# Performance work log

Hardware: AMD Instinct MI355X
Metric: run time of the kernel (lower is better)

The kernel has to match this reference:

```python
import jax, jax.numpy as jnp
import numpy as np

# geomloss SamplesLoss('sinkhorn', p=1, blur=0.05, diameter=10) equivalents
BLUR = 0.05        # final epsilon (p=1 -> eps = blur**1)
DIAMETER = 10.0    # starting epsilon for eps-scaling
SCALING = 0.5      # geomloss default annealing ratio
N_POINTS = 32
SPACE_DIM = 8      # emb_dim // n_points = 256 // 32


def _eps_schedule():
    eps, e = [], DIAMETER
    while e > BLUR:
        eps.append(e)
        e *= SCALING
    eps.append(BLUR)
    return eps  # static python list -> unrolled under jit


def _cost(x, y):
    # p=1 ground cost: euclidean distance. x:[B,n,d], y:[B,m,d] -> [B,n,m]
    sq = (jnp.sum(x * x, -1)[:, :, None] + jnp.sum(y * y, -1)[:, None, :]
          - 2.0 * jnp.einsum('bnd,bmd->bnm', x, y))
    return jnp.sqrt(jnp.maximum(sq, 0.0) + 1e-8)


def _softmin(eps, C, h):
    # -eps * logsumexp_j( log(1/n) + (h_j - C_ij)/eps ), uniform weights
    n = C.shape[-1]
    return -eps * jax.nn.logsumexp((h[:, None, :] - C) / eps - jnp.log(n), axis=-1)


def _sinkhorn_div(x, y):
    # Debiased Sinkhorn divergence with epsilon scaling (log-domain, symmetric
    # averaged updates, as in geomloss). x, y: [B, n, d] -> [B]
    C_xy = _cost(x, y)
    C_yx = jnp.swapaxes(C_xy, 1, 2)
    C_xx = _cost(x, x)
    C_yy = _cost(y, y)
    B, n, _ = C_xy.shape
    z = jnp.zeros((B, n), x.dtype)
    f_ab, g_ba, f_aa, g_bb = z, z, z, z
    for eps in _eps_schedule():
        ft = _softmin(eps, C_xy, g_ba)
        gt = _softmin(eps, C_yx, f_ab)
        fat = _softmin(eps, C_xx, f_aa)
        gbt = _softmin(eps, C_yy, g_bb)
        f_ab = 0.5 * (f_ab + ft)
        g_ba = 0.5 * (g_ba + gt)
        f_aa = 0.5 * (f_aa + fat)
        g_bb = 0.5 * (g_bb + gbt)
    return jnp.mean(f_ab - f_aa, axis=1) + jnp.mean(g_ba - g_bb, axis=1)


def _encode(x, edge_index, W):
    # simple mean-aggregation GCN layer standing in for the generic encoder
    src, dst = edge_index[0], edge_index[1]
    N = x.shape[0]
    agg = jax.ops.segment_sum(x[src], dst, num_segments=N)
    deg = jax.ops.segment_sum(jnp.ones((src.shape[0],), x.dtype), dst, num_segments=N)
    return (agg / jnp.maximum(deg, 1.0)[:, None]) @ W  # [N, emb_dim]


def setup_inputs() -> dict:
    key = jax.random.key(0)
    k1, k2, k3, k4, k5 = jax.random.split(key, 5)
    N, F, EMB = 100000, 128, 256
    return {
        'x': jax.random.normal(k1, (N, F), dtype=jnp.float32),
        'edge_index': jax.random.randint(k2, (2, 1600000), 0, N, dtype=jnp.int64),
        'edges_pos': jax.random.randint(k3, (2, 30000), 0, N, dtype=jnp.int64),
        'edges_neg': jax.random.randint(k4, (2, 30000), 0, N, dtype=jnp.int64),
        'W': jax.random.normal(k5, (F, EMB), dtype=jnp.float32) * (1.0 / np.sqrt(F)),
    }


def reference(x, edge_index, edges_pos, edges_neg, W):
    z = _encode(x, edge_index, W)

    def energy(edges):  # -score_pairs = sinkhorn divergence
        zx = z[edges[0]].reshape(-1, N_POINTS, SPACE_DIM)
        zy = z[edges[1]].reshape(-1, N_POINTS, SPACE_DIM)
        return _sinkhorn_div(zx, zy)

    pos_energy = energy(edges_pos)
    neg_energy = energy(edges_neg)
    margin = jnp.maximum(1.0 - neg_energy, 0.0)
    return jnp.mean(pos_energy ** 2) + jnp.mean(margin ** 2)
```

## Files before the change

### kernel.cpp

```cpp
#include <hip/hip_runtime.h>
#include <hip/hip_bf16.h>


__global__ __launch_bounds__(256) void sge_count(
    const int* __restrict__ dst, int* __restrict__ cnt, int nE) {
  int e = blockIdx.x * 256 + threadIdx.x;
  if (e >= nE) return;
  atomicAdd(&cnt[dst[e]], 1);
}

__global__ __launch_bounds__(256) void sge_blocksum(
    const int* __restrict__ cnt, int* __restrict__ bsum, int N) {
  int i = blockIdx.x * 256 + threadIdx.x;
  int v = (i < N) ? cnt[i] : 0;
#pragma unroll
  for (int o = 1; o < 64; o <<= 1) v += __shfl_xor(v, o);
  __shared__ int ws[4];
  int lane = threadIdx.x & 63, wid = threadIdx.x >> 6;
  if (lane == 0) ws[wid] = v;
  __syncthreads();
  if (threadIdx.x == 0)
    bsum[blockIdx.x] = ws[0] + ws[1] + ws[2] + ws[3];
}

__global__ __launch_bounds__(64) void sge_scan_top(
    int* __restrict__ bsum, int* __restrict__ offs, int nb, int N, int nE) {
  int lane = threadIdx.x;
  int carry = 0;
  for (int base = 0; base < nb; base += 64) {
    int i = base + lane;
    int v = (i < nb) ? bsum[i] : 0;
    int s = v;
#pragma unroll
    for (int o = 1; o < 64; o <<= 1) {
      int t = __shfl_up(s, o);
      if (lane >= o) s += t;
    }
    if (i < nb) bsum[i] = carry + s - v;
    carry += __shfl(s, 63);
  }
  if (lane == 0) offs[N] = nE;
}

__global__ __launch_bounds__(256) void sge_scan_block(
    const int* __restrict__ cnt, const int* __restrict__ bsum,
    int* __restrict__ offs, int* __restrict__ pos, int N) {
  int i = blockIdx.x * 256 + threadIdx.x;
  int v = (i < N) ? cnt[i] : 0;
  int lane = threadIdx.x & 63, wid = threadIdx.x >> 6;
  int s = v;
#pragma unroll
  for (int o = 1; o < 64; o <<= 1) {
    int t = __shfl_up(s, o);
    if (lane >= o) s += t;
  }
  __shared__ int ws[4];
  if (lane == 63) ws[wid] = s;
  __syncthreads();
  int wbase = 0;
  for (int w = 0; w < wid; ++w) wbase += ws[w];
  if (i < N) {
    int o = bsum[blockIdx.x] + wbase + s - v;
    offs[i] = o;
    pos[i] = o;
  }
}

__global__ __launch_bounds__(256) void sge_fill(
    const int* __restrict__ src, const int* __restrict__ dst,
    int* __restrict__ pos, int* __restrict__ sorted_src, int nE) {
  int e = blockIdx.x * 256 + threadIdx.x;
  if (e >= nE) return;
  int p = atomicAdd(&pos[dst[e]], 1);
  sorted_src[p] = src[e];
}

__global__ __launch_bounds__(256) void sge_gather(
    const float* __restrict__ x, const int* __restrict__ sorted_src,
    const int* __restrict__ offs, float* __restrict__ agg, int N) {
  int node = blockIdx.x * 4 + (threadIdx.x >> 6);
  int lane = threadIdx.x & 63;
  int h = lane >> 5;
  int c4 = (lane & 31) << 2;
  if (node >= N) return;
  int e0 = offs[node], e1 = offs[node + 1];
  float4 A = {0.f, 0.f, 0.f, 0.f}, B = {0.f, 0.f, 0.f, 0.f};
  int e = e0 + h;
  for (; e + 2 < e1; e += 4) {
    int s0 = sorted_src[e];
    int s1 = sorted_src[e + 2];
    float4 v0 = *(const float4*)&x[(size_t)s0 * 128 + c4];
    float4 v1 = *(const float4*)&x[(size_t)s1 * 128 + c4];
    A.x += v0.x; A.y += v0.y; A.z += v0.z; A.w += v0.w;
    B.x += v1.x; B.y += v1.y; B.z += v1.z; B.w += v1.w;
  }
  if (e < e1) {
    float4 v0 = *(const float4*)&x[(size_t)sorted_src[e] * 128 + c4];
    A.x += v0.x; A.y += v0.y; A.z += v0.z; A.w += v0.w;
  }
  float4 S;
  S.x = A.x + B.x; S.y = A.y + B.y; S.z = A.z + B.z; S.w = A.w + B.w;
  S.x += __shfl_xor(S.x, 32);
  S.y += __shfl_xor(S.y, 32);
  S.z += __shfl_xor(S.z, 32);
  S.w += __shfl_xor(S.w, 32);
  if (h == 0) {
    float inv = 1.0f / fmaxf((float)(e1 - e0), 1.0f);
    float4 r;
    r.x = S.x * inv; r.y = S.y * inv; r.z = S.z * inv; r.w = S.w * inv;
    *(float4*)&agg[(size_t)node * 128 + c4] = r;
  }
}

__global__ __launch_bounds__(256) void sge_gemm(
    const float* __restrict__ agg, const float* __restrict__ W,
    float* __restrict__ z) {
  __shared__ float xs[32][128];
  int n0 = blockIdx.x * 32;
  int t = threadIdx.x;
#pragma unroll
  for (int i = 0; i < 16; ++i) {
    int idx = t + i * 256;
    int r = idx >> 7;
    int c = idx & 127;
    xs[r][c] = agg[(long long)(n0 + r) * 128 + c];
  }
  __syncthreads();
  int wv = t >> 6, lane = t & 63;
  int r0 = wv * 8;
  float acc[8][4];
#pragma unroll
  for (int r = 0; r < 8; ++r)
#pragma unroll
    for (int q = 0; q < 4; ++q) acc[r][q] = 0.f;
  for (int k = 0; k < 128; k += 4) {
    float4 xv[8];
#pragma unroll
    for (int r = 0; r < 8; ++r) xv[r] = *(const float4*)&xs[r0 + r][k];
#pragma unroll
    for (int kk = 0; kk < 4; ++kk) {
      const float* Wr = W + (k + kk) * 256 + lane;
      float w0 = Wr[0], w1 = Wr[64], w2 = Wr[128], w3 = Wr[192];
#pragma unroll
      for (int r = 0; r < 8; ++r) {
        float xk = (kk == 0) ? xv[r].x
                 : (kk == 1) ? xv[r].y
                 : (kk == 2) ? xv[r].z : xv[r].w;
        acc[r][0] = fmaf(xk, w0, acc[r][0]);
        acc[r][1] = fmaf(xk, w1, acc[r][1]);
        acc[r][2] = fmaf(xk, w2, acc[r][2]);
        acc[r][3] = fmaf(xk, w3, acc[r][3]);
      }
    }
  }
#pragma unroll
  for (int r = 0; r < 8; ++r) {
    float* zr = z + (long long)(n0 + r0 + r) * 256 + lane;
#pragma unroll
    for (int q = 0; q < 4; ++q) zr[q * 64] = acc[r][q];
  }
}

template <int CTRL>
__device__ __forceinline__ float dpp_max(float x) {
  int r = __builtin_amdgcn_update_dpp(__float_as_int(x), __float_as_int(x),
                                      CTRL, 0xF, 0xF, false);
  return fmaxf(x, __int_as_float(r));
}
template <int CTRL>
__device__ __forceinline__ float dpp_add(float x) {
  int r = __builtin_amdgcn_update_dpp(0, __float_as_int(x), CTRL, 0xF, 0xF, true);
  return x + __int_as_float(r);
}

__global__ __launch_bounds__(256, 4) void sge_energy(
    const float* __restrict__ z, const int* __restrict__ ep,
    const int* __restrict__ en, float* __restrict__ partial, int nP) {
  __shared__ __align__(16) float Ebuf[2][2][64];
  __shared__ __align__(16) float Nbuf[2][2][64];
  __shared__ float red[2][2];

  int t = threadIdx.x;
  int pl = t >> 7;
  int tp = t & 127;
  int w = tp >> 6;
  int l = tp & 63;
  int row = l & 31;
  int own = l & 32;

  int pair = blockIdx.x * 2 + pl;
  bool isPos = pair < nP;
  int idx = isPos ? pair : pair - nP;
  const int* E = isPos ? ep : en;
  int na = E[idx], nb = E[idx + nP];

  const float* zrow = z + (size_t)(own ? nb : na) * 256 + row * 8;
  float4 r0 = ((const float4*)zrow)[0];
  float4 r1 = ((const float4*)zrow)[1];
  float xr[8];
  xr[0] = r0.x; xr[1] = r0.y; xr[2] = r0.z; xr[3] = r0.w;
  xr[4] = r1.x; xr[5] = r1.y; xr[6] = r1.z; xr[7] = r1.w;

  float nself = xr[0] * xr[0];
  nself = fmaf(xr[1], xr[1], nself); nself = fmaf(xr[2], xr[2], nself);
  nself = fmaf(xr[3], xr[3], nself); nself = fmaf(xr[4], xr[4], nself);
  nself = fmaf(xr[5], xr[5], nself); nself = fmaf(xr[6], xr[6], nself);
  nself = fmaf(xr[7], xr[7], nself);
  Nbuf[pl][w][l] = nself;
  __builtin_amdgcn_wave_barrier();

  bool colIsX = (w == 0) ? (own != 0) : (own == 0);
  const float4* zc = (const float4*)(z + (size_t)(colIsX ? na : nb) * 256);
  int rb = (w == 0) ? (own ^ 32) : own;
  const float* Nw = Nbuf[pl][w] + rb;

  const float RLNE = 1.44269504088896340736f;
  const float LN2 = 0.69314718055994530942f;
  const float LN32 = 3.46573590279972654709f;
  const float K20 = RLNE / 10.0f;
  const float NK28 = -RLNE / 0.05f;

  float C[32], V[32];
#pragma unroll
  for (int jq = 0; jq < 8; ++jq) {
    float4 nj4 = ((const float4*)Nw)[jq];
    float4 a[8];
#pragma unroll
    for (int k = 0; k < 4; ++k) {
      a[2 * k] = zc[8 * jq + 2 * k];
      a[2 * k + 1] = zc[8 * jq + 2 * k + 1];
    }
#pragma unroll
    for (int k = 0; k < 4; ++k) {
      int j = jq * 4 + k;
      float4 a0 = a[2 * k], a1 = a[2 * k + 1];
      float d = xr[0] * a0.x;
      d = fmaf(xr[1], a0.y, d); d = fmaf(xr[2], a0.z, d);
      d = fmaf(xr[3], a0.w, d); d = fmaf(xr[4], a1.x, d);
      d = fmaf(xr[5], a1.y, d); d = fmaf(xr[6], a1.z, d);
      d = fmaf(xr[7], a1.w, d);
      float nj = (k == 0) ? nj4.x : (k == 1) ? nj4.y : (k == 2) ? nj4.z : nj4.w;
      float sq = fmaf(-2.0f, d, nself + nj);
      float Cv = __builtin_amdgcn_sqrtf(fmaxf(sq, 0.0f) + 1e-8f);
      C[j] = Cv;
      V[j] = __builtin_amdgcn_exp2f(-Cv * K20);
    }
  }

  float* Ew = Ebuf[pl][w];

  float P = 0.0f;
  float epsv = 10.0f;

#pragma unroll 1
  for (int it = 0; it < 9; ++it) {
    float eps = (it == 8) ? 0.05f : epsv;
    float k2 = RLNE / eps;
    float eln2 = eps * LN2;
    float c32 = eps * LN32;

    if (it == 8) {
#pragma unroll
      for (int j = 0; j < 32; ++j)
        V[j] = __builtin_amdgcn_exp2f(C[j] * NK28);
    } else if (it > 0) {
#pragma unroll
      for (int j = 0; j < 32; ++j) V[j] *= V[j];
    }

    float mOwn, mRead;
    if (it >= 7) {
      float m = P;
      m = dpp_max<0x111>(m);
      m = dpp_max<0x112>(m);
      m = dpp_max<0x114>(m);
      m = dpp_max<0x118>(m);
      m = dpp_max<0x142>(m);
      float g0 = __int_as_float(__builtin_amdgcn_readlane(__float_as_int(m), 31));
      float g1 = __int_as_float(__builtin_amdgcn_readlane(__float_as_int(m), 63));
      mOwn = own ? g1 : g0;
      mRead = (w == 0) ? (own ? g0 : g1) : mOwn;
    } else {
      mOwn = 0.0f;
      mRead = 0.0f;
    }

    Ew[l] = __builtin_amdgcn_exp2f((P - mOwn) * k2);
    __builtin_amdgcn_wave_barrier();

    float s0 = 0.f, s1 = 0.f, s2 = 0.f, s3 = 0.f;
#pragma unroll
    for (int jq = 0; jq < 8; ++jq) {
      float4 Ev = ((const float4*)(Ew + rb))[jq];
      s0 = fmaf(Ev.x, V[4 * jq + 0], s0);
      s1 = fmaf(Ev.y, V[4 * jq + 1], s1);
      s2 = fmaf(Ev.z, V[4 * jq + 2], s2);
      s3 = fmaf(Ev.w, V[4 * jq + 3], s3);
    }
    float s = fmaxf((s0 + s1) + (s2 + s3), 1e-37f);
    __builtin_amdgcn_wave_barrier();

    P = 0.5f * (P + (c32 - mRead - eln2 * __builtin_amdgcn_logf(s)));
    epsv *= 0.5f;
  }

  float d = P;
  d = dpp_add<0x111>(d);
  d = dpp_add<0x112>(d);
  d = dpp_add<0x114>(d);
  d = dpp_add<0x118>(d);
  d = dpp_add<0x142>(d);
  float s31 = __int_as_float(__builtin_amdgcn_readlane(__float_as_int(d), 31));
  float s63 = __int_as_float(__builtin_amdgcn_readlane(__float_as_int(d), 63));
  if (l == 0) red[pl][w] = s31 + s63;
  __syncthreads();
  if (t == 0) {
    float tot = 0.0f;
#pragma unroll
    for (int q = 0; q < 2; ++q) {
      int pr = blockIdx.x * 2 + q;
      float e = (red[q][0] - red[q][1]) * (1.0f / 32.0f);
      float term;
      if (pr < nP) {
        term = e * e;
      } else {
        float mm = fmaxf(1.0f - e, 0.0f);
        term = mm * mm;
      }
      tot += term;
    }
    partial[blockIdx.x] = tot;
  }
}

__global__ __launch_bounds__(1024) void sge_reduce(
    const float* __restrict__ partial, int n, float invnP,
    float* __restrict__ out) {
  __shared__ float ws[16];
  float s = 0.0f;
  for (int i = threadIdx.x; i < n; i += 1024) s += partial[i];
#pragma unroll
  for (int o = 1; o < 64; o <<= 1) s += __shfl_xor(s, o);
  if ((threadIdx.x & 63) == 0) ws[threadIdx.x >> 6] = s;
  __syncthreads();
  if (threadIdx.x == 0) {
    float tt = 0.0f;
#pragma unroll
    for (int q = 0; q < 16; ++q) tt += ws[q];
    out[0] = tt * invnP;
  }
}

extern "C" void kernel_launch(void* const* d_in, const int* in_sizes, int n_in,
                              void* d_out, int out_size, void* d_ws, size_t ws_size,
                              hipStream_t stream) {
  const float* x  = (const float*)d_in[0];
  const int*   ei = (const int*)d_in[1];
  const int*   ep = (const int*)d_in[2];
  const int*   en = (const int*)d_in[3];
  const float* W  = (const float*)d_in[4];
  float* out = (float*)d_out;

  int N  = in_sizes[0] / 128;
  int nE = in_sizes[1] / 2;
  int nP = in_sizes[2] / 2;

  size_t zBytes   = (size_t)N * 256 * sizeof(float);
  size_t aggBytes = (size_t)N * 128 * sizeof(float);
  if (ws_size < zBytes + aggBytes) return;

  char* ws = (char*)d_ws;
  float* z   = (float*)ws;
  float* agg = (float*)(ws + zBytes);

  int* cnt        = (int*)ws;
  int* offs       = cnt + N;
  int* pos        = offs + N + 1;
  int* bsum       = pos + N;
  int* sorted_src = bsum + 4096;

  float* partial = agg;

  int nb = (N + 255) / 256;

  hipMemsetAsync(cnt, 0, (size_t)N * sizeof(int), stream);

  const int* src = ei;
  const int* dst = ei + nE;

  int eb = (nE + 255) / 256;
  sge_count<<<eb, 256, 0, stream>>>(dst, cnt, nE);
  sge_blocksum<<<nb, 256, 0, stream>>>(cnt, bsum, N);
  sge_scan_top<<<1, 64, 0, stream>>>(bsum, offs, nb, N, nE);
  sge_scan_block<<<nb, 256, 0, stream>>>(cnt, bsum, offs, pos, N);
  sge_fill<<<eb, 256, 0, stream>>>(src, dst, pos, sorted_src, nE);
  sge_gather<<<(N + 3) / 4, 256, 0, stream>>>(x, sorted_src, offs, agg, N);

  sge_gemm<<<(N + 31) / 32, 256, 0, stream>>>(agg, W, z);

  sge_energy<<<nP, 256, 0, stream>>>(z, ep, en, partial, nP);
  sge_reduce<<<1, 1024, 0, stream>>>(partial, nP, 1.0f / (float)nP, out);
}
```

Before: 690.9 us.

## Process one pair per wave computing both cross and self kernels per lane

```diff
diff --git a/kernel.cpp b/kernel.cpp
--- a/kernel.cpp
+++ b/kernel.cpp
@@ -172,25 +172,30 @@
   int r = __builtin_amdgcn_update_dpp(0, __float_as_int(x), CTRL, 0xF, 0xF, true);
   return x + __int_as_float(r);
 }
+__device__ __forceinline__ float rdlane(float v, int lane) {
+  return __int_as_float(__builtin_amdgcn_readlane(__float_as_int(v), lane));
+}
 
 __global__ __launch_bounds__(256, 4) void sge_energy(
     const float* __restrict__ z, const int* __restrict__ ep,
     const int* __restrict__ en, float* __restrict__ partial, int nP) {
-  __shared__ __align__(16) float Ebuf[2][2][64];
-  __shared__ __align__(16) float Nbuf[2][2][64];
-  __shared__ float red[2][2];
+  __shared__ __align__(16) float EbA[4][64];
+  __shared__ __align__(16) float EbB[4][64];
+  __shared__ __align__(16) float Nbuf[4][64];
+  __shared__ float red[4];
 
   int t = threadIdx.x;
-  int pl = t >> 7;
-  int tp = t & 127;
-  int w = tp >> 6;
-  int l = tp & 63;
+  int wv = t >> 6;
+  int l = t & 63;
   int row = l & 31;
   int own = l & 32;
 
-  int pair = blockIdx.x * 2 + pl;
-  bool isPos = pair < nP;
-  int idx = isPos ? pair : pair - nP;
+  int n2 = 2 * nP;
+  int pair = blockIdx.x * 4 + wv;
+  bool live = pair < n2;
+  int pr = live ? pair : 0;
+  bool isPos = pr < nP;
+  int idx = isPos ? pr : pr - nP;
   const int* E = isPos ? ep : en;
   int na = E[idx], nb = E[idx + nP];
 
@@ -206,50 +211,57 @@
   nself = fmaf(xr[3], xr[3], nself); nself = fmaf(xr[4], xr[4], nself);
   nself = fmaf(xr[5], xr[5], nself); nself = fmaf(xr[6], xr[6], nself);
   nself = fmaf(xr[7], xr[7], nself);
-  Nbuf[pl][w][l] = nself;
+  Nbuf[wv][l] = nself;
   __builtin_amdgcn_wave_barrier();
 
-  bool colIsX = (w == 0) ? (own != 0) : (own == 0);
-  const float4* zc = (const float4*)(z + (size_t)(colIsX ? na : nb) * 256);
-  int rb = (w == 0) ? (own ^ 32) : own;
-  const float* Nw = Nbuf[pl][w] + rb;
+  const float4* zcA = (const float4*)(z + (size_t)(own ? na : nb) * 256);
+  const float4* zcB = (const float4*)(z + (size_t)(own ? nb : na) * 256);
+  int rbA = own ^ 32;
+  int rbB = own;
+  const float* NwA = Nbuf[wv] + rbA;
+  const float* NwB = Nbuf[wv] + rbB;
 
   const float RLNE = 1.44269504088896340736f;
   const float LN2 = 0.69314718055994530942f;
   const float LN32 = 3.46573590279972654709f;
   const float K20 = RLNE / 10.0f;
-  const float NK28 = -RLNE / 0.05f;
-
-  float C[32], V[32];
+
+  float VA[32], VB[32];
 #pragma unroll
   for (int jq = 0; jq < 8; ++jq) {
-    float4 nj4 = ((const float4*)Nw)[jq];
-    float4 a[8];
-#pragma unroll
-    for (int k = 0; k < 4; ++k) {
-      a[2 * k] = zc[8 * jq + 2 * k];
-      a[2 * k + 1] = zc[8 * jq + 2 * k + 1];
-    }
+    float4 njA = ((const float4*)NwA)[jq];
+    float4 njB = ((const float4*)NwB)[jq];
 #pragma unroll
     for (int k = 0; k < 4; ++k) {
       int j = jq * 4 + k;
-      float4 a0 = a[2 * k], a1 = a[2 * k + 1];
-      float d = xr[0] * a0.x;
-      d = fmaf(xr[1], a0.y, d); d = fmaf(xr[2], a0.z, d);
-      d = fmaf(xr[3], a0.w, d); d = fmaf(xr[4], a1.x, d);
-      d = fmaf(xr[5], a1.y, d); d = fmaf(xr[6], a1.z, d);
-      d = fmaf(xr[7], a1.w, d);
-      float nj = (k == 0) ? nj4.x : (k == 1) ? nj4.y : (k == 2) ? nj4.z : nj4.w;
-      float sq = fmaf(-2.0f, d, nself + nj);
-      float Cv = __builtin_amdgcn_sqrtf(fmaxf(sq, 0.0f) + 1e-8f);
-      C[j] = Cv;
-      V[j] = __builtin_amdgcn_exp2f(-Cv * K20);
-    }
-  }
-
-  float* Ew = Ebuf[pl][w];
-
-  float P = 0.0f;
+      float4 a0 = zcA[2 * j];
+      float4 a1 = zcA[2 * j + 1];
+      float4 b0 = zcB[2 * j];
+      float4 b1 = zcB[2 * j + 1];
+      float dA = xr[0] * a0.x;
+      float dB = xr[0] * b0.x;
+      dA = fmaf(xr[1], a0.y, dA); dB = fmaf(xr[1], b0.y, dB);
+      dA = fmaf(xr[2], a0.z, dA); dB = fmaf(xr[2], b0.z, dB);
+      dA = fmaf(xr[3], a0.w, dA); dB = fmaf(xr[3], b0.w, dB);
+      dA = fmaf(xr[4], a1.x, dA); dB = fmaf(xr[4], b1.x, dB);
+      dA = fmaf(xr[5], a1.y, dA); dB = fmaf(xr[5], b1.y, dB);
+      dA = fmaf(xr[6], a1.z, dA); dB = fmaf(xr[6], b1.z, dB);
+      dA = fmaf(xr[7], a1.w, dA); dB = fmaf(xr[7], b1.w, dB);
+      float nA = (k == 0) ? njA.x : (k == 1) ? njA.y : (k == 2) ? njA.z : njA.w;
+      float nB = (k == 0) ? njB.x : (k == 1) ? njB.y : (k == 2) ? njB.z : njB.w;
+      float sqA = fmaf(-2.0f, dA, nself + nA);
+      float sqB = fmaf(-2.0f, dB, nself + nB);
+      float CA = __builtin_amdgcn_sqrtf(fmaxf(sqA, 0.0f) + 1e-8f);
+      float CB = __builtin_amdgcn_sqrtf(fmaxf(sqB, 0.0f) + 1e-8f);
+      VA[j] = __builtin_amdgcn_exp2f(-CA * K20);
+      VB[j] = __builtin_amdgcn_exp2f(-CB * K20);
+    }
+  }
+
+  float* EA = EbA[wv];
+  float* EB = EbB[wv];
+
+  float PA = 0.0f, PB = 0.0f;
   float epsv = 10.0f;
 
 #pragma unroll 1
@@ -261,76 +273,88 @@
 
     if (it == 8) {
 #pragma unroll
-      for (int j = 0; j < 32; ++j)
-        V[j] = __builtin_amdgcn_exp2f(C[j] * NK28);
+      for (int j = 0; j < 32; ++j) {
+        VA[j] = __builtin_amdgcn_exp2f(1.5625f * __builtin_amdgcn_logf(VA[j]));
+        VB[j] = __builtin_amdgcn_exp2f(1.5625f * __builtin_amdgcn_logf(VB[j]));
+      }
     } else if (it > 0) {
 #pragma unroll
-      for (int j = 0; j < 32; ++j) V[j] *= V[j];
-    }
-
-    float mOwn, mRead;
+      for (int j = 0; j < 32; ++j) {
+        VA[j] *= VA[j];
+        VB[j] *= VB[j];
+      }
+    }
+
+    float mOwnA, mReadA, mOwnB;
     if (it >= 7) {
-      float m = P;
-      m = dpp_max<0x111>(m);
-      m = dpp_max<0x112>(m);
-      m = dpp_max<0x114>(m);
-      m = dpp_max<0x118>(m);
-      m = dpp_max<0x142>(m);
-      float g0 = __int_as_float(__builtin_amdgcn_readlane(__float_as_int(m), 31));
-      float g1 = __int_as_float(__builtin_amdgcn_readlane(__float_as_int(m), 63));
-      mOwn = own ? g1 : g0;
-      mRead = (w == 0) ? (own ? g0 : g1) : mOwn;
+      float mA = PA, mB = PB;
+      mA = dpp_max<0x111>(mA); mB = dpp_max<0x111>(mB);
+      mA = dpp_max<0x112>(mA); mB = dpp_max<0x112>(mB);
+      mA = dpp_max<0x114>(mA); mB = dpp_max<0x114>(mB);
+      mA = dpp_max<0x118>(mA); mB = dpp_max<0x118>(mB);
+      mA = dpp_max<0x142>(mA); mB = dpp_max<0x142>(mB);
+      float gA0 = rdlane(mA, 31), gA1 = rdlane(mA, 63);
+      float gB0 = rdlane(mB, 31), gB1 = rdlane(mB, 63);
+      mOwnA = own ? gA1 : gA0;
+      mReadA = own ? gA0 : gA1;
+      mOwnB = own ? gB1 : gB0;
     } else {
-      mOwn = 0.0f;
-      mRead = 0.0f;
-    }
-
-    Ew[l] = __builtin_amdgcn_exp2f((P - mOwn) * k2);
+      mOwnA = mReadA = 0.0f;
+      mOwnB = 0.0f;
+    }
+
+    EA[l] = __builtin_amdgcn_exp2f((PA - mOwnA) * k2);
+    EB[l] = __builtin_amdgcn_exp2f((PB - mOwnB) * k2);
     __builtin_amdgcn_wave_barrier();
 
-    float s0 = 0.f, s1 = 0.f, s2 = 0.f, s3 = 0.f;
+    float sA0 = 0.f, sA1 = 0.f, sA2 = 0.f, sA3 = 0.f;
+    float sB0 = 0.f, sB1 = 0.f, sB2 = 0.f, sB3 = 0.f;
 #pragma unroll
     for (int jq = 0; jq < 8; ++jq) {
-      float4 Ev = ((const float4*)(Ew + rb))[jq];
-      s0 = fmaf(Ev.x, V[4 * jq + 0], s0);
-      s1 = fmaf(Ev.y, V[4 * jq + 1], s1);
-      s2 = fmaf(Ev.z, V[4 * jq + 2], s2);
-      s3 = fmaf(Ev.w, V[4 * jq + 3], s3);
-    }
-    float s = fmaxf((s0 + s1) + (s2 + s3), 1e-37f);
+      float4 EvA = ((const float4*)(EA + rbA))[jq];
+      float4 EvB = ((const float4*)(EB + rbB))[jq];
+      sA0 = fmaf(EvA.x, VA[4 * jq + 0], sA0);
+      sB0 = fmaf(EvB.x, VB[4 * jq + 0], sB0);
+      sA1 = fmaf(EvA.y, VA[4 * jq + 1], sA1);
+      sB1 = fmaf(EvB.y, VB[4 * jq + 1], sB1);
+      sA2 = fmaf(EvA.z, VA[4 * jq + 2], sA2);
+      sB2 = fmaf(EvB.z, VB[4 * jq + 2], sB2);
+      sA3 = fmaf(EvA.w, VA[4 * jq + 3], sA3);
+      sB3 = fmaf(EvB.w, VB[4 * jq + 3], sB3);
+    }
+    float sA = fmaxf((sA0 + sA1) + (sA2 + sA3), 1e-37f);
+    float sB = fmaxf((sB0 + sB1) + (sB2 + sB3), 1e-37f);
     __builtin_amdgcn_wave_barrier();
 
-    P = 0.5f * (P + (c32 - mRead - eln2 * __builtin_amdgcn_logf(s)));
+    PA = 0.5f * (PA + (c32 - mReadA - eln2 * __builtin_amdgcn_logf(sA)));
+    PB = 0.5f * (PB + (c32 - mOwnB - eln2 * __builtin_amdgcn_logf(sB)));
     epsv *= 0.5f;
   }
 
-  float d = P;
-  d = dpp_add<0x111>(d);
-  d = dpp_add<0x112>(d);
-  d = dpp_add<0x114>(d);
-  d = dpp_add<0x118>(d);
-  d = dpp_add<0x142>(d);
-  float s31 = __int_as_float(__builtin_amdgcn_readlane(__float_as_int(d), 31));
-  float s63 = __int_as_float(__builtin_amdgcn_readlane(__float_as_int(d), 63));
-  if (l == 0) red[pl][w] = s31 + s63;
-  __syncthreads();
-  if (t == 0) {
-    float tot = 0.0f;
-#pragma unroll
-    for (int q = 0; q < 2; ++q) {
-      int pr = blockIdx.x * 2 + q;
-      float e = (red[q][0] - red[q][1]) * (1.0f / 32.0f);
-      float term;
-      if (pr < nP) {
+  float dA = PA, dB = PB;
+  dA = dpp_add<0x111>(dA); dB = dpp_add<0x111>(dB);
+  dA = dpp_add<0x112>(dA); dB = dpp_add<0x112>(dB);
+  dA = dpp_add<0x114>(dA); dB = dpp_add<0x114>(dB);
+  dA = dpp_add<0x118>(dA); dB = dpp_add<0x118>(dB);
+  dA = dpp_add<0x142>(dA); dB = dpp_add<0x142>(dB);
+  float sumA = rdlane(dA, 31) + rdlane(dA, 63);
+  float sumB = rdlane(dB, 31) + rdlane(dB, 63);
+  if (l == 0) {
+    float term = 0.0f;
+    if (live) {
+      float e = (sumA - sumB) * (1.0f / 32.0f);
+      if (isPos) {
         term = e * e;
       } else {
         float mm = fmaxf(1.0f - e, 0.0f);
         term = mm * mm;
       }
-      tot += term;
-    }
-    partial[blockIdx.x] = tot;
-  }
+    }
+    red[wv] = term;
+  }
+  __syncthreads();
+  if (t == 0)
+    partial[blockIdx.x] = (red[0] + red[1]) + (red[2] + red[3]);
 }
 
 __global__ __launch_bounds__(1024) void sge_reduce(
@@ -398,6 +422,7 @@
 
   sge_gemm<<<(N + 31) / 32, 256, 0, stream>>>(agg, W, z);
 
-  sge_energy<<<nP, 256, 0, stream>>>(z, ep, en, partial, nP);
-  sge_reduce<<<1, 1024, 0, stream>>>(partial, nP, 1.0f / (float)nP, out);
-}
+  int eblocks = (2 * nP + 3) / 4;
+  sge_energy<<<eblocks, 256, 0, stream>>>(z, ep, en, partial, nP);
+  sge_reduce<<<1, 1024, 0, stream>>>(partial, eblocks, 1.0f / (float)nP, out);
+}
```

After: 1.313 ms. 90.1% more time.

## Split Sinkhorn rows across lane pairs and drop stored cost matrix

Applied to the files above, without the earlier changes.

```diff
diff --git a/kernel.cpp b/kernel.cpp
--- a/kernel.cpp
+++ b/kernel.cpp
@@ -172,21 +172,25 @@
   int r = __builtin_amdgcn_update_dpp(0, __float_as_int(x), CTRL, 0xF, 0xF, true);
   return x + __int_as_float(r);
 }
+__device__ __forceinline__ float rdlane(float v, int lane) {
+  return __int_as_float(__builtin_amdgcn_readlane(__float_as_int(v), lane));
+}
 
 __global__ __launch_bounds__(256, 4) void sge_energy(
     const float* __restrict__ z, const int* __restrict__ ep,
     const int* __restrict__ en, float* __restrict__ partial, int nP) {
-  __shared__ __align__(16) float Ebuf[2][2][64];
-  __shared__ __align__(16) float Nbuf[2][2][64];
+  __shared__ __align__(16) float EbA[4][32];
+  __shared__ __align__(16) float EbB[4][32];
+  __shared__ __align__(16) float Nbuf[4][64];
   __shared__ float red[2][2];
 
   int t = threadIdx.x;
-  int pl = t >> 7;
-  int tp = t & 127;
-  int w = tp >> 6;
-  int l = tp & 63;
-  int row = l & 31;
-  int own = l & 32;
+  int wv = t >> 6;
+  int pl = wv >> 1;
+  int w = wv & 1;
+  int l = t & 63;
+  int row = l >> 1;
+  int ch = l & 1;
 
   int pair = blockIdx.x * 2 + pl;
   bool isPos = pair < nP;
@@ -194,62 +198,80 @@
   const int* E = isPos ? ep : en;
   int na = E[idx], nb = E[idx + nP];
 
-  const float* zrow = z + (size_t)(own ? nb : na) * 256 + row * 8;
-  float4 r0 = ((const float4*)zrow)[0];
-  float4 r1 = ((const float4*)zrow)[1];
-  float xr[8];
-  xr[0] = r0.x; xr[1] = r0.y; xr[2] = r0.z; xr[3] = r0.w;
-  xr[4] = r1.x; xr[5] = r1.y; xr[6] = r1.z; xr[7] = r1.w;
-
-  float nself = xr[0] * xr[0];
-  nself = fmaf(xr[1], xr[1], nself); nself = fmaf(xr[2], xr[2], nself);
-  nself = fmaf(xr[3], xr[3], nself); nself = fmaf(xr[4], xr[4], nself);
-  nself = fmaf(xr[5], xr[5], nself); nself = fmaf(xr[6], xr[6], nself);
-  nself = fmaf(xr[7], xr[7], nself);
-  Nbuf[pl][w][l] = nself;
+  const float* zx = z + (size_t)na * 256;
+  const float* zy = z + (size_t)nb * 256;
+
+  float xrow[8], yrow[8];
+  {
+    float4 a0 = ((const float4*)(zx + row * 8))[0];
+    float4 a1 = ((const float4*)(zx + row * 8))[1];
+    float4 b0 = ((const float4*)(zy + row * 8))[0];
+    float4 b1 = ((const float4*)(zy + row * 8))[1];
+    xrow[0] = a0.x; xrow[1] = a0.y; xrow[2] = a0.z; xrow[3] = a0.w;
+    xrow[4] = a1.x; xrow[5] = a1.y; xrow[6] = a1.z; xrow[7] = a1.w;
+    yrow[0] = b0.x; yrow[1] = b0.y; yrow[2] = b0.z; yrow[3] = b0.w;
+    yrow[4] = b1.x; yrow[5] = b1.y; yrow[6] = b1.z; yrow[7] = b1.w;
+  }
+  float nxr = xrow[0] * xrow[0];
+  float nyr = yrow[0] * yrow[0];
+#pragma unroll
+  for (int d = 1; d < 8; ++d) {
+    nxr = fmaf(xrow[d], xrow[d], nxr);
+    nyr = fmaf(yrow[d], yrow[d], nyr);
+  }
+  Nbuf[wv][row] = nxr;
+  Nbuf[wv][32 + row] = nyr;
   __builtin_amdgcn_wave_barrier();
 
-  bool colIsX = (w == 0) ? (own != 0) : (own == 0);
-  const float4* zc = (const float4*)(z + (size_t)(colIsX ? na : nb) * 256);
-  int rb = (w == 0) ? (own ^ 32) : own;
-  const float* Nw = Nbuf[pl][w] + rb;
+  const float4* colsA = (const float4*)((w == 0) ? zy : zx);
+  const float4* colsB = (const float4*)((w == 0) ? zx : zy);
+  const float* NcA = (w == 0) ? (Nbuf[wv] + 32) : Nbuf[wv];
+  const float* NcB = (w == 0) ? Nbuf[wv] : (Nbuf[wv] + 32);
 
   const float RLNE = 1.44269504088896340736f;
   const float LN2 = 0.69314718055994530942f;
   const float LN32 = 3.46573590279972654709f;
   const float K20 = RLNE / 10.0f;
-  const float NK28 = -RLNE / 0.05f;
-
-  float C[32], V[32];
-#pragma unroll
-  for (int jq = 0; jq < 8; ++jq) {
-    float4 nj4 = ((const float4*)Nw)[jq];
-    float4 a[8];
+
+  float VA[16], VB[16];
+#pragma unroll
+  for (int jq = 0; jq < 4; ++jq) {
+    float4 nA4 = ((const float4*)(NcA + ch * 16))[jq];
+    float4 nB4 = ((const float4*)(NcB + ch * 16))[jq];
 #pragma unroll
     for (int k = 0; k < 4; ++k) {
-      a[2 * k] = zc[8 * jq + 2 * k];
-      a[2 * k + 1] = zc[8 * jq + 2 * k + 1];
-    }
-#pragma unroll
-    for (int k = 0; k < 4; ++k) {
-      int j = jq * 4 + k;
-      float4 a0 = a[2 * k], a1 = a[2 * k + 1];
-      float d = xr[0] * a0.x;
-      d = fmaf(xr[1], a0.y, d); d = fmaf(xr[2], a0.z, d);
-      d = fmaf(xr[3], a0.w, d); d = fmaf(xr[4], a1.x, d);
-      d = fmaf(xr[5], a1.y, d); d = fmaf(xr[6], a1.z, d);
-      d = fmaf(xr[7], a1.w, d);
-      float nj = (k == 0) ? nj4.x : (k == 1) ? nj4.y : (k == 2) ? nj4.z : nj4.w;
-      float sq = fmaf(-2.0f, d, nself + nj);
-      float Cv = __builtin_amdgcn_sqrtf(fmaxf(sq, 0.0f) + 1e-8f);
-      C[j] = Cv;
-      V[j] = __builtin_amdgcn_exp2f(-Cv * K20);
-    }
-  }
-
-  float* Ew = Ebuf[pl][w];
-
-  float P = 0.0f;
+      int jj = jq * 4 + k;
+      int j = ch * 16 + jj;
+      float4 a0 = colsA[2 * j];
+      float4 a1 = colsA[2 * j + 1];
+      float4 b0 = colsB[2 * j];
+      float4 b1 = colsB[2 * j + 1];
+      float dA = xrow[0] * a0.x;
+      float dB = yrow[0] * b0.x;
+      dA = fmaf(xrow[1], a0.y, dA); dB = fmaf(yrow[1], b0.y, dB);
+      dA = fmaf(xrow[2], a0.z, dA); dB = fmaf(yrow[2], b0.z, dB);
+      dA = fmaf(xrow[3], a0.w, dA); dB = fmaf(yrow[3], b0.w, dB);
+      dA = fmaf(xrow[4], a1.x, dA); dB = fmaf(yrow[4], b1.x, dB);
+      dA = fmaf(xrow[5], a1.y, dA); dB = fmaf(yrow[5], b1.y, dB);
+      dA = fmaf(xrow[6], a1.z, dA); dB = fmaf(yrow[6], b1.z, dB);
+      dA = fmaf(xrow[7], a1.w, dA); dB = fmaf(yrow[7], b1.w, dB);
+      float nA = (k == 0) ? nA4.x : (k == 1) ? nA4.y : (k == 2) ? nA4.z : nA4.w;
+      float nB = (k == 0) ? nB4.x : (k == 1) ? nB4.y : (k == 2) ? nB4.z : nB4.w;
+      float sqA = fmaf(-2.0f, dA, nxr + nA);
+      float sqB = fmaf(-2.0f, dB, nyr + nB);
+      float CA = __builtin_amdgcn_sqrtf(fmaxf(sqA, 0.0f) + 1e-8f);
+      float CB = __builtin_amdgcn_sqrtf(fmaxf(sqB, 0.0f) + 1e-8f);
+      VA[jj] = __builtin_amdgcn_exp2f(-CA * K20);
+      VB[jj] = __builtin_amdgcn_exp2f(-CB * K20);
+    }
+  }
+
+  float* EAw = EbA[wv];
+  float* EBw = EbB[wv];
+  const float* ErdA = (w == 0) ? EBw : EAw;
+  const float* ErdB = (w == 0) ? EAw : EBw;
+
+  float PA = 0.0f, PB = 0.0f;
   float epsv = 10.0f;
 
 #pragma unroll 1
@@ -261,65 +283,82 @@
 
     if (it == 8) {
 #pragma unroll
-      for (int j = 0; j < 32; ++j)
-        V[j] = __builtin_amdgcn_exp2f(C[j] * NK28);
+      for (int j = 0; j < 16; ++j) {
+        VA[j] = __builtin_amdgcn_exp2f(1.5625f * __builtin_amdgcn_logf(VA[j]));
+        VB[j] = __builtin_amdgcn_exp2f(1.5625f * __builtin_amdgcn_logf(VB[j]));
+      }
     } else if (it > 0) {
 #pragma unroll
-      for (int j = 0; j < 32; ++j) V[j] *= V[j];
-    }
-
-    float mOwn, mRead;
+      for (int j = 0; j < 16; ++j) {
+        VA[j] *= VA[j];
+        VB[j] *= VB[j];
+      }
+    }
+
+    float mA, mB;
     if (it >= 7) {
-      float m = P;
-      m = dpp_max<0x111>(m);
-      m = dpp_max<0x112>(m);
-      m = dpp_max<0x114>(m);
-      m = dpp_max<0x118>(m);
-      m = dpp_max<0x142>(m);
-      float g0 = __int_as_float(__builtin_amdgcn_readlane(__float_as_int(m), 31));
-      float g1 = __int_as_float(__builtin_amdgcn_readlane(__float_as_int(m), 63));
-      mOwn = own ? g1 : g0;
-      mRead = (w == 0) ? (own ? g0 : g1) : mOwn;
+      float a = PA, b = PB;
+      a = dpp_max<0x111>(a); b = dpp_max<0x111>(b);
+      a = dpp_max<0x112>(a); b = dpp_max<0x112>(b);
+      a = dpp_max<0x114>(a); b = dpp_max<0x114>(b);
+      a = dpp_max<0x118>(a); b = dpp_max<0x118>(b);
+      a = dpp_max<0x142>(a); b = dpp_max<0x142>(b);
+      mA = fmaxf(rdlane(a, 31), rdlane(a, 63));
+      mB = fmaxf(rdlane(b, 31), rdlane(b, 63));
     } else {
-      mOwn = 0.0f;
-      mRead = 0.0f;
-    }
-
-    Ew[l] = __builtin_amdgcn_exp2f((P - mOwn) * k2);
+      mA = 0.0f;
+      mB = 0.0f;
+    }
+
+    EAw[row] = __builtin_amdgcn_exp2f((PA - mA) * k2);
+    EBw[row] = __builtin_amdgcn_exp2f((PB - mB) * k2);
     __builtin_amdgcn_wave_barrier();
 
-    float s0 = 0.f, s1 = 0.f, s2 = 0.f, s3 = 0.f;
-#pragma unroll
-    for (int jq = 0; jq < 8; ++jq) {
-      float4 Ev = ((const float4*)(Ew + rb))[jq];
-      s0 = fmaf(Ev.x, V[4 * jq + 0], s0);
-      s1 = fmaf(Ev.y, V[4 * jq + 1], s1);
-      s2 = fmaf(Ev.z, V[4 * jq + 2], s2);
-      s3 = fmaf(Ev.w, V[4 * jq + 3], s3);
-    }
-    float s = fmaxf((s0 + s1) + (s2 + s3), 1e-37f);
+    float sA0 = 0.f, sA1 = 0.f, sA2 = 0.f, sA3 = 0.f;
+    float sB0 = 0.f, sB1 = 0.f, sB2 = 0.f, sB3 = 0.f;
+#pragma unroll
+    for (int jq = 0; jq < 4; ++jq) {
+      float4 EvA = ((const float4*)(ErdA + ch * 16))[jq];
+      float4 EvB = ((const float4*)(ErdB + ch * 16))[jq];
+      sA0 = fmaf(EvA.x, VA[4 * jq + 0], sA0);
+      sB0 = fmaf(EvB.x, VB[4 * jq + 0], sB0);
+      sA1 = fmaf(EvA.y, VA[4 * jq + 1], sA1);
+      sB1 = fmaf(EvB.y, VB[4 * jq + 1], sB1);
+      sA2 = fmaf(EvA.z, VA[4 * jq + 2], sA2);
+      sB2 = fmaf(EvB.z, VB[4 * jq + 2], sB2);
+      sA3 = fmaf(EvA.w, VA[4 * jq + 3], sA3);
+      sB3 = fmaf(EvB.w, VB[4 * jq + 3], sB3);
+    }
+    float sA = (sA0 + sA1) + (sA2 + sA3);
+    float sB = (sB0 + sB1) + (sB2 + sB3);
+    sA = dpp_add<0xB1>(sA);
+    sB = dpp_add<0xB1>(sB);
+    sA = fmaxf(sA, 1e-37f);
+    sB = fmaxf(sB, 1e-37f);
     __builtin_amdgcn_wave_barrier();
 
-    P = 0.5f * (P + (c32 - mRead - eln2 * __builtin_amdgcn_logf(s)));
+    float mUA = (w == 0) ? mB : mA;
+    float mUB = (w == 0) ? mA : mB;
+    PA = 0.5f * (PA + (c32 - mUA - eln2 * __builtin_amdgcn_logf(sA)));
+    PB = 0.5f * (PB + (c32 - mUB - eln2 * __builtin_amdgcn_logf(sB)));
     epsv *= 0.5f;
   }
 
-  float d = P;
+  float d = PA + PB;
   d = dpp_add<0x111>(d);
   d = dpp_add<0x112>(d);
   d = dpp_add<0x114>(d);
   d = dpp_add<0x118>(d);
   d = dpp_add<0x142>(d);
-  float s31 = __int_as_float(__builtin_amdgcn_readlane(__float_as_int(d), 31));
-  float s63 = __int_as_float(__builtin_amdgcn_readlane(__float_as_int(d), 63));
-  if (l == 0) red[pl][w] = s31 + s63;
+  float sum = rdlane(d, 31) + rdlane(d, 63);
+  if (l == 0) red[pl][w] = sum;
   __syncthreads();
   if (t == 0) {
     float tot = 0.0f;
 #pragma unroll
     for (int q = 0; q < 2; ++q) {
       int pr = blockIdx.x * 2 + q;
-      float e = (red[q][0] - red[q][1]) * (1.0f / 32.0f);
+      float e = (red[q][0] - red[q][1]) * (1.0f / 64.0f);
       float term;
       if (pr < nP) {
         term = e * e;
@@ -398,6 +437,7 @@
 
   sge_gemm<<<(N + 31) / 32, 256, 0, stream>>>(agg, W, z);
 
-  sge_energy<<<nP, 256, 0, stream>>>(z, ep, en, partial, nP);
-  sge_reduce<<<1, 1024, 0, stream>>>(partial, nP, 1.0f / (float)nP, out);
-}
+  int eblocks = nP;
+  sge_energy<<<eblocks, 256, 0, stream>>>(z, ep, en, partial, nP);
+  sge_reduce<<<1, 1024, 0, stream>>>(partial, eblocks, 1.0f / (float)nP, out);
+}
```

After: 871.8 us. 1.26x slower.

## Fuse neighbor mean-aggregation gather into the GEMM shared-memory tile load

Applied to the files above, without the earlier changes.

```diff
diff --git a/kernel.cpp b/kernel.cpp
--- a/kernel.cpp
+++ b/kernel.cpp
@@ -75,57 +75,41 @@
   sorted_src[p] = src[e];
 }
 
-__global__ __launch_bounds__(256) void sge_gather(
+__global__ __launch_bounds__(256) void sge_gemm(
     const float* __restrict__ x, const int* __restrict__ sorted_src,
-    const int* __restrict__ offs, float* __restrict__ agg, int N) {
-  int node = blockIdx.x * 4 + (threadIdx.x >> 6);
-  int lane = threadIdx.x & 63;
-  int h = lane >> 5;
-  int c4 = (lane & 31) << 2;
-  if (node >= N) return;
-  int e0 = offs[node], e1 = offs[node + 1];
-  float4 A = {0.f, 0.f, 0.f, 0.f}, B = {0.f, 0.f, 0.f, 0.f};
-  int e = e0 + h;
-  for (; e + 2 < e1; e += 4) {
-    int s0 = sorted_src[e];
-    int s1 = sorted_src[e + 2];
-    float4 v0 = *(const float4*)&x[(size_t)s0 * 128 + c4];
-    float4 v1 = *(const float4*)&x[(size_t)s1 * 128 + c4];
-    A.x += v0.x; A.y += v0.y; A.z += v0.z; A.w += v0.w;
-    B.x += v1.x; B.y += v1.y; B.z += v1.z; B.w += v1.w;
-  }
-  if (e < e1) {
-    float4 v0 = *(const float4*)&x[(size_t)sorted_src[e] * 128 + c4];
-    A.x += v0.x; A.y += v0.y; A.z += v0.z; A.w += v0.w;
-  }
-  float4 S;
-  S.x = A.x + B.x; S.y = A.y + B.y; S.z = A.z + B.z; S.w = A.w + B.w;
-  S.x += __shfl_xor(S.x, 32);
-  S.y += __shfl_xor(S.y, 32);
-  S.z += __shfl_xor(S.z, 32);
-  S.w += __shfl_xor(S.w, 32);
-  if (h == 0) {
-    float inv = 1.0f / fmaxf((float)(e1 - e0), 1.0f);
-    float4 r;
-    r.x = S.x * inv; r.y = S.y * inv; r.z = S.z * inv; r.w = S.w * inv;
-    *(float4*)&agg[(size_t)node * 128 + c4] = r;
-  }
-}
-
-__global__ __launch_bounds__(256) void sge_gemm(
-    const float* __restrict__ agg, const float* __restrict__ W,
+    const int* __restrict__ offs, const float* __restrict__ W,
     float* __restrict__ z) {
   __shared__ float xs[32][128];
   int n0 = blockIdx.x * 32;
   int t = threadIdx.x;
-#pragma unroll
-  for (int i = 0; i < 16; ++i) {
-    int idx = t + i * 256;
-    int r = idx >> 7;
-    int c = idx & 127;
-    xs[r][c] = agg[(long long)(n0 + r) * 128 + c];
-  }
-  __syncthreads();
+
+  {
+    int r = t >> 3;
+    int c0 = (t & 7) << 4;
+    int node = n0 + r;
+    int e0 = offs[node], e1 = offs[node + 1];
+    float4 a0 = {0.f, 0.f, 0.f, 0.f}, a1 = {0.f, 0.f, 0.f, 0.f};
+    float4 a2 = {0.f, 0.f, 0.f, 0.f}, a3 = {0.f, 0.f, 0.f, 0.f};
+    for (int e = e0; e < e1; ++e) {
+      int s = sorted_src[e];
+      const float4* xr = (const float4*)&x[(size_t)s * 128 + c0];
+      float4 v0 = xr[0], v1 = xr[1], v2 = xr[2], v3 = xr[3];
+      a0.x += v0.x; a0.y += v0.y; a0.z += v0.z; a0.w += v0.w;
+      a1.x += v1.x; a1.y += v1.y; a1.z += v1.z; a1.w += v1.w;
+      a2.x += v2.x; a2.y += v2.y; a2.z += v2.z; a2.w += v2.w;
+      a3.x += v3.x; a3.y += v3.y; a3.z += v3.z; a3.w += v3.w;
+    }
+    float inv = 1.0f / fmaxf((float)(e1 - e0), 1.0f);
+    float4* xw = (float4*)&xs[r][c0];
+    float4 w0, w1, w2, w3;
+    w0.x = a0.x * inv; w0.y = a0.y * inv; w0.z = a0.z * inv; w0.w = a0.w * inv;
+    w1.x = a1.x * inv; w1.y = a1.y * inv; w1.z = a1.z * inv; w1.w = a1.w * inv;
+    w2.x = a2.x * inv; w2.y = a2.y * inv; w2.z = a2.z * inv; w2.w = a2.w * inv;
+    w3.x = a3.x * inv; w3.y = a3.y * inv; w3.z = a3.z * inv; w3.w = a3.w * inv;
+    xw[0] = w0; xw[1] = w1; xw[2] = w2; xw[3] = w3;
+  }
+  __syncthreads();
+
   int wv = t >> 6, lane = t & 63;
   int r0 = wv * 8;
   float acc[8][4];
@@ -370,16 +354,15 @@
   if (ws_size < zBytes + aggBytes) return;
 
   char* ws = (char*)d_ws;
-  float* z   = (float*)ws;
-  float* agg = (float*)(ws + zBytes);
-
-  int* cnt        = (int*)ws;
+  float* z = (float*)ws;
+
+  int* base2      = (int*)(ws + zBytes);
+  int* cnt        = base2;
   int* offs       = cnt + N;
   int* pos        = offs + N + 1;
   int* bsum       = pos + N;
   int* sorted_src = bsum + 4096;
-
-  float* partial = agg;
+  float* partial  = (float*)(sorted_src + nE);
 
   int nb = (N + 255) / 256;
 
@@ -394,9 +377,8 @@
   sge_scan_top<<<1, 64, 0, stream>>>(bsum, offs, nb, N, nE);
   sge_scan_block<<<nb, 256, 0, stream>>>(cnt, bsum, offs, pos, N);
   sge_fill<<<eb, 256, 0, stream>>>(src, dst, pos, sorted_src, nE);
-  sge_gather<<<(N + 3) / 4, 256, 0, stream>>>(x, sorted_src, offs, agg, N);
-
-  sge_gemm<<<(N + 31) / 32, 256, 0, stream>>>(agg, W, z);
+
+  sge_gemm<<<(N + 31) / 32, 256, 0, stream>>>(x, sorted_src, offs, W, z);
 
   sge_energy<<<nP, 256, 0, stream>>>(z, ep, en, partial, nP);
   sge_reduce<<<1, 1024, 0, stream>>>(partial, nP, 1.0f / (float)nP, out);
```

Result: faster. 644.2 us, median of 2 (-6.7%).
